# Kernel optimization log

Hardware: AMD Instinct MI355X
Metric: run time of the kernel (lower is better)

## Reference

```python
import jax, jax.numpy as jnp
import numpy as np

N_NODES = 100000
N_EDGES = 1600000
F_IN = 128
HID = 128
N_GRAPHS = 2048


def setup_inputs() -> dict:
    key = jax.random.key(0)
    ks = jax.random.split(key, 12)
    x = jax.random.normal(ks[0], (N_NODES, F_IN), dtype=jnp.float32)
    edge_index = jax.random.randint(ks[1], (2, N_EDGES), 0, N_NODES, dtype=jnp.int64)
    batch = jnp.sort(jax.random.randint(ks[2], (N_NODES,), 0, N_GRAPHS, dtype=jnp.int64))
    def glorot(k, fan_in, fan_out):
        s = jnp.sqrt(6.0 / (fan_in + fan_out)).astype(jnp.float32)
        return jax.random.uniform(k, (fan_in, fan_out), jnp.float32, -s, s)
    W1 = glorot(ks[3], F_IN, HID); b1 = jnp.zeros((HID,), jnp.float32)
    W2 = glorot(ks[4], HID, HID);  b2 = jnp.zeros((HID,), jnp.float32)
    W3 = glorot(ks[5], HID, HID);  b3 = jnp.zeros((HID,), jnp.float32)
    W4 = glorot(ks[6], HID, HID);  b4 = jnp.zeros((HID,), jnp.float32)
    return {"x": x, "W1": W1, "b1": b1, "W2": W2, "b2": b2,
            "W3": W3, "b3": b3, "W4": W4, "b4": b4,
            "edge_index": edge_index, "batch": batch}


def _gcn_norm(edge_index, n_nodes):
    # add self-loops, symmetric normalization: norm_e = d^{-1/2}[row] * d^{-1/2}[col]
    loop = jnp.arange(n_nodes, dtype=edge_index.dtype)
    row = jnp.concatenate([edge_index[0], loop])  # source
    col = jnp.concatenate([edge_index[1], loop])  # target
    deg = jax.ops.segment_sum(jnp.ones_like(col, dtype=jnp.float32), col,
                              num_segments=n_nodes)
    dis = jnp.where(deg > 0, jax.lax.rsqrt(jnp.maximum(deg, 1.0)), 0.0)
    norm = dis[row] * dis[col]
    return row, col, norm


def _gcn_conv(x, W, b, row, col, norm, n_nodes):
    h = x @ W                                   # [N, d_out]
    msg = norm[:, None] * h[row]                # gather + scale, [E+N, d_out]
    out = jax.ops.segment_sum(msg, col, num_segments=n_nodes)
    return out + b


def reference(x, W1, b1, W2, b2, W3, b3, W4, b4, edge_index, batch):
    n = x.shape[0]
    row, col, norm = _gcn_norm(edge_index, n)
    h = jax.nn.relu(_gcn_conv(x, W1, b1, row, col, norm, n))
    h = jax.nn.relu(_gcn_conv(h, W2, b2, row, col, norm, n))
    h = jax.nn.relu(_gcn_conv(h, W3, b3, row, col, norm, n))
    h = jax.nn.relu(_gcn_conv(h, W4, b4, row, col, norm, n))
    # global mean pool over graphs in the batch
    sums = jax.ops.segment_sum(h, batch, num_segments=N_GRAPHS)
    cnts = jax.ops.segment_sum(jnp.ones((n,), jnp.float32), batch,
                               num_segments=N_GRAPHS)
    return sums / jnp.maximum(cnts, 1.0)[:, None]
```

## Files before the change

kernel.cpp:

```cpp
#include <hip/hip_runtime.h>
#include <hip/hip_bf16.h>
#include <hip/hip_fp16.h>

typedef _Float16 half8 __attribute__((ext_vector_type(8)));
typedef _Float16 h2    __attribute__((ext_vector_type(2)));
typedef float    f32x4 __attribute__((ext_vector_type(4)));


__global__ void count_deg_k(const int* __restrict__ col,
                            unsigned int* __restrict__ deg, int E) {
    int e = blockIdx.x * blockDim.x + threadIdx.x;
    if (e < E) atomicAdd(&deg[col[e]], 1u);
}

__global__ void dis_k(const unsigned int* __restrict__ deg,
                      float* __restrict__ dis, int N) {
    int i = blockIdx.x * blockDim.x + threadIdx.x;
    if (i < N) dis[i] = rsqrtf((float)(deg[i] + 1u));
}

__global__ void scan1_k(const unsigned int* __restrict__ deg,
                        int* __restrict__ out, int* __restrict__ bsum, int N) {
    __shared__ int lds[256];
    int t = threadIdx.x;
    int base = blockIdx.x * 1024 + t * 4;
    int v0 = (base + 0 < N) ? (int)deg[base + 0] : 0;
    int v1 = (base + 1 < N) ? (int)deg[base + 1] : 0;
    int v2 = (base + 2 < N) ? (int)deg[base + 2] : 0;
    int v3 = (base + 3 < N) ? (int)deg[base + 3] : 0;
    lds[t] = v0 + v1 + v2 + v3;
    __syncthreads();
    for (int off = 1; off < 256; off <<= 1) {
        int x = lds[t];
        int y = (t >= off) ? lds[t - off] : 0;
        __syncthreads();
        lds[t] = x + y;
        __syncthreads();
    }
    int excl = (t == 0) ? 0 : lds[t - 1];
    if (base + 0 < N) out[base + 0] = excl;
    excl += v0;
    if (base + 1 < N) out[base + 1] = excl;
    excl += v1;
    if (base + 2 < N) out[base + 2] = excl;
    excl += v2;
    if (base + 3 < N) out[base + 3] = excl;
    if (t == 255) bsum[blockIdx.x] = lds[255];
}

__global__ void scan2_k(const int* __restrict__ bsum, int* __restrict__ boff, int nb) {
    __shared__ int lds[256];
    int t = threadIdx.x;
    lds[t] = (t < nb) ? bsum[t] : 0;
    __syncthreads();
    for (int off = 1; off < 256; off <<= 1) {
        int x = lds[t];
        int y = (t >= off) ? lds[t - off] : 0;
        __syncthreads();
        lds[t] = x + y;
        __syncthreads();
    }
    boff[t] = (t == 0) ? 0 : lds[t - 1];
}

__global__ void scan3_k(int* __restrict__ row_ptr, int* __restrict__ cursor,
                        const int* __restrict__ boff, int N, int E) {
    int i = blockIdx.x * blockDim.x + threadIdx.x;
    if (i < N) {
        int v = row_ptr[i] + boff[i >> 10];
        row_ptr[i] = v;
        cursor[i]  = v;
    }
    if (i == N) row_ptr[N] = E;
}

__global__ void fill_k(const int* __restrict__ row,
                       const int* __restrict__ col,
                       int* __restrict__ cursor, int* __restrict__ csr_row, int E) {
    int e = blockIdx.x * blockDim.x + threadIdx.x;
    if (e < E) {
        int c = col[e];
        int p = atomicAdd(&cursor[c], 1);
        csr_row[p] = row[e];
    }
}

__global__ void cnt_k(const int* __restrict__ batch,
                      unsigned int* __restrict__ cnt, int N) {
    int i = blockIdx.x * blockDim.x + threadIdx.x;
    if (i < N) atomicAdd(&cnt[batch[i]], 1u);
}

__global__ void wtcast_k(const float* __restrict__ W, _Float16* __restrict__ Wt) {
    int t = blockIdx.x * 256 + threadIdx.x;
    int k = t >> 7, n = t & 127;
    Wt[n * 128 + k] = (_Float16)W[t];
}

template<bool F32IN>
__global__ __launch_bounds__(256) void gemm_mfma_k(const void* __restrict__ Ain,
                                                   const _Float16* __restrict__ Wt,
                                                   const float* __restrict__ dis,
                                                   _Float16* __restrict__ H, int N) {
    int wave = threadIdx.x >> 6, l = threadIdx.x & 63;
    int lr = l & 15, lk = l >> 4;
    int row0 = blockIdx.x * 128 + wave * 32;

    half8 a[2][4];
#pragma unroll
    for (int m = 0; m < 2; ++m) {
#pragma unroll
        for (int s = 0; s < 4; ++s) {
            int r = row0 + m * 16 + lr;
            int k0 = s * 32 + lk * 8;
            half8 t;
            if (r < N) {
                if constexpr (F32IN) {
                    const float* ap = (const float*)Ain + (size_t)r * 128 + k0;
                    float4 u0 = *(const float4*)ap;
                    float4 u1 = *(const float4*)(ap + 4);
                    t[0] = (_Float16)u0.x; t[1] = (_Float16)u0.y;
                    t[2] = (_Float16)u0.z; t[3] = (_Float16)u0.w;
                    t[4] = (_Float16)u1.x; t[5] = (_Float16)u1.y;
                    t[6] = (_Float16)u1.z; t[7] = (_Float16)u1.w;
                } else {
                    t = *(const half8*)((const _Float16*)Ain + (size_t)r * 128 + k0);
                }
            } else {
#pragma unroll
                for (int i = 0; i < 8; ++i) t[i] = (_Float16)0.0f;
            }
            a[m][s] = t;
        }
    }

    f32x4 acc[2][8];
#pragma unroll
    for (int m = 0; m < 2; ++m)
#pragma unroll
        for (int nt = 0; nt < 8; ++nt)
#pragma unroll
            for (int r = 0; r < 4; ++r) acc[m][nt][r] = 0.0f;

#pragma unroll
    for (int nt = 0; nt < 8; ++nt) {
        half8 b[4];
#pragma unroll
        for (int s = 0; s < 4; ++s)
            b[s] = *(const half8*)(Wt + (size_t)(nt * 16 + lr) * 128 + s * 32 + lk * 8);
#pragma unroll
        for (int m = 0; m < 2; ++m)
#pragma unroll
            for (int s = 0; s < 4; ++s)
                acc[m][nt] = __builtin_amdgcn_mfma_f32_16x16x32_f16(a[m][s], b[s],
                                                                    acc[m][nt], 0, 0, 0);
    }

#pragma unroll
    for (int m = 0; m < 2; ++m) {
        int   orow[4];
        float dv[4];
#pragma unroll
        for (int r = 0; r < 4; ++r) {
            orow[r] = row0 + m * 16 + lk * 4 + r;
            dv[r]   = (orow[r] < N) ? dis[orow[r]] : 0.0f;
        }
#pragma unroll
        for (int nt = 0; nt < 8; ++nt)
#pragma unroll
            for (int r = 0; r < 4; ++r)
                if (orow[r] < N)
                    H[(size_t)orow[r] * 128 + nt * 16 + lr] =
                        (_Float16)(acc[m][nt][r] * dv[r]);
    }
}

template<bool POOL>
__global__ __launch_bounds__(256) void agg_h_k(const _Float16* __restrict__ Hd,
                                               const int* __restrict__ row_ptr,
                                               const int* __restrict__ csr_row,
                                               const float* __restrict__ dis,
                                               const float* __restrict__ bias,
                                               _Float16* __restrict__ Hout,
                                               const int* __restrict__ batch,
                                               float* __restrict__ pout, int N) {
    int wid  = (int)((blockIdx.x * (size_t)blockDim.x + threadIdx.x) >> 6);
    int lane = threadIdx.x & 63;
    if (wid >= N) return;
    int beg = row_ptr[wid], end = row_ptr[wid + 1];
    float di = dis[wid];
    const _Float16* hp = Hd + lane * 2;

    h2 self = *(const h2*)(hp + (size_t)wid * 128);
    float ax = (float)self[0], ay = (float)self[1];

    int j = beg;
    for (; j + 4 <= end; j += 4) {
        int s0 = csr_row[j], s1 = csr_row[j + 1], s2 = csr_row[j + 2], s3 = csr_row[j + 3];
        h2 v0 = *(const h2*)(hp + (size_t)s0 * 128);
        h2 v1 = *(const h2*)(hp + (size_t)s1 * 128);
        h2 v2 = *(const h2*)(hp + (size_t)s2 * 128);
        h2 v3 = *(const h2*)(hp + (size_t)s3 * 128);
        ax += (float)v0[0] + (float)v1[0] + (float)v2[0] + (float)v3[0];
        ay += (float)v0[1] + (float)v1[1] + (float)v2[1] + (float)v3[1];
    }
    for (; j < end; ++j) {
        int s = csr_row[j];
        h2 v = *(const h2*)(hp + (size_t)s * 128);
        ax += (float)v[0];
        ay += (float)v[1];
    }

    float bx = bias[lane * 2], by = bias[lane * 2 + 1];
    float ox = fmaxf(fmaf(di, ax, bx), 0.0f);
    float oy = fmaxf(fmaf(di, ay, by), 0.0f);

    if constexpr (POOL) {
        int g = batch[wid];
        atomicAdd(&pout[(size_t)g * 128 + lane * 2 + 0], ox);
        atomicAdd(&pout[(size_t)g * 128 + lane * 2 + 1], oy);
    } else {
        h2 o;
        o[0] = (_Float16)ox;
        o[1] = (_Float16)oy;
        *(h2*)(Hout + (size_t)wid * 128 + lane * 2) = o;
    }
}

__global__ void fin_k(float* __restrict__ out, const unsigned int* __restrict__ cnt,
                      int total) {
    int i = blockIdx.x * blockDim.x + threadIdx.x;
    if (i < total) out[i] = out[i] / fmaxf((float)cnt[i >> 7], 1.0f);
}

extern "C" void kernel_launch(void* const* d_in, const int* in_sizes, int n_in,
                              void* d_out, int out_size, void* d_ws, size_t ws_size,
                              hipStream_t stream) {
    const float* x  = (const float*)d_in[0];
    const float* W1 = (const float*)d_in[1]; const float* b1 = (const float*)d_in[2];
    const float* W2 = (const float*)d_in[3]; const float* b2 = (const float*)d_in[4];
    const float* W3 = (const float*)d_in[5]; const float* b3 = (const float*)d_in[6];
    const float* W4 = (const float*)d_in[7]; const float* b4 = (const float*)d_in[8];
    const int* eidx  = (const int*)d_in[9];
    const int* batch = (const int*)d_in[10];

    int N = in_sizes[0] / 128;
    int E = in_sizes[9] / 2;
    const int* erow = eidx;
    const int* ecol = eidx + E;

    char* ws = (char*)d_ws;
    size_t off = 0;
    auto alloc = [&](size_t bytes) -> void* {
        void* p = ws + off;
        off = (off + bytes + 255) & ~(size_t)255;
        return p;
    };
    unsigned int* deg    = (unsigned int*)alloc((size_t)N * 4);
    float*        dis    = (float*)alloc((size_t)N * 4);
    int*          rowp   = (int*)alloc((size_t)(N + 1) * 4);
    int*          cursor = (int*)alloc((size_t)N * 4);
    int*          bsum   = (int*)alloc(1024);
    int*          boff   = (int*)alloc(1024);
    unsigned int* cnt    = (unsigned int*)alloc(2048 * 4);
    int*          csr    = (int*)alloc((size_t)E * 4);
    _Float16*     Wt1    = (_Float16*)alloc(128 * 128 * 2);
    _Float16*     Wt2    = (_Float16*)alloc(128 * 128 * 2);
    _Float16*     Wt3    = (_Float16*)alloc(128 * 128 * 2);
    _Float16*     Wt4    = (_Float16*)alloc(128 * 128 * 2);
    _Float16*     hA     = (_Float16*)alloc((size_t)N * 128 * 2);
    _Float16*     hB     = (_Float16*)alloc((size_t)N * 128 * 2);
    (void)ws_size;

    hipMemsetAsync(deg, 0, (size_t)N * 4, stream);
    hipMemsetAsync(cnt, 0, 2048 * 4, stream);
    hipMemsetAsync(d_out, 0, (size_t)out_size * 4, stream);

    const int B = 256;
    count_deg_k<<<(E + B - 1) / B, B, 0, stream>>>(ecol, deg, E);
    dis_k<<<(N + B - 1) / B, B, 0, stream>>>(deg, dis, N);
    int nb = (N + 1023) / 1024;
    scan1_k<<<nb, 256, 0, stream>>>(deg, rowp, bsum, N);
    scan2_k<<<1, 256, 0, stream>>>(bsum, boff, nb);
    scan3_k<<<(N + 1 + B - 1) / B, B, 0, stream>>>(rowp, cursor, boff, N, E);
    fill_k<<<(E + B - 1) / B, B, 0, stream>>>(erow, ecol, cursor, csr, E);
    cnt_k<<<(N + B - 1) / B, B, 0, stream>>>(batch, cnt, N);
    wtcast_k<<<64, 256, 0, stream>>>(W1, Wt1);
    wtcast_k<<<64, 256, 0, stream>>>(W2, Wt2);
    wtcast_k<<<64, 256, 0, stream>>>(W3, Wt3);
    wtcast_k<<<64, 256, 0, stream>>>(W4, Wt4);

    int gb = (N + 127) / 128;
    int ab = (N + 3) / 4;

    gemm_mfma_k<true ><<<gb, 256, 0, stream>>>(x,  Wt1, dis, hA, N);
    agg_h_k<false><<<ab, 256, 0, stream>>>(hA, rowp, csr, dis, b1, hB, batch, nullptr, N);
    gemm_mfma_k<false><<<gb, 256, 0, stream>>>(hB, Wt2, dis, hA, N);
    agg_h_k<false><<<ab, 256, 0, stream>>>(hA, rowp, csr, dis, b2, hB, batch, nullptr, N);
    gemm_mfma_k<false><<<gb, 256, 0, stream>>>(hB, Wt3, dis, hA, N);
    agg_h_k<false><<<ab, 256, 0, stream>>>(hA, rowp, csr, dis, b3, hB, batch, nullptr, N);
    gemm_mfma_k<false><<<gb, 256, 0, stream>>>(hB, Wt4, dis, hA, N);
    agg_h_k<true ><<<ab, 256, 0, stream>>>(hA, rowp, csr, dis, b4, nullptr, batch,
                                           (float*)d_out, N);

    fin_k<<<(out_size + B - 1) / B, B, 0, stream>>>((float*)d_out, cnt, out_size);
}
```

Before: 774.6 us.

## Fuse aggregation with next layer GEMM and merge setup kernels

Each layer's neighbour aggregation is now fused with the following layer's MFMA GEMM: a block aggregates 64 nodes into shared memory, then multiplies by the next weight matrix and writes the scaled result. This removes the intermediate activation write and re-read and the separate GEMM launches. Setup kernels are also merged: degree and batch counting share one kernel, dis is computed inside the scan, and the four weight casts become one launch. The fused kernel processes 16 nodes serially per wave with fewer blocks, which may reduce latency hiding in the gather phase.

```diff
diff --git a/kernel.cpp b/kernel.cpp
--- a/kernel.cpp
+++ b/kernel.cpp
@@ -7,20 +7,17 @@
 typedef float    f32x4 __attribute__((ext_vector_type(4)));
 
 
-__global__ void count_deg_k(const int* __restrict__ col,
-                            unsigned int* __restrict__ deg, int E) {
+__global__ void count2_k(const int* __restrict__ col, unsigned int* __restrict__ deg,
+                         const int* __restrict__ batch, unsigned int* __restrict__ cnt,
+                         int E, int N) {
     int e = blockIdx.x * blockDim.x + threadIdx.x;
     if (e < E) atomicAdd(&deg[col[e]], 1u);
-}
-
-__global__ void dis_k(const unsigned int* __restrict__ deg,
-                      float* __restrict__ dis, int N) {
-    int i = blockIdx.x * blockDim.x + threadIdx.x;
-    if (i < N) dis[i] = rsqrtf((float)(deg[i] + 1u));
+    if (e < N) atomicAdd(&cnt[batch[e]], 1u);
 }
 
 __global__ void scan1_k(const unsigned int* __restrict__ deg,
-                        int* __restrict__ out, int* __restrict__ bsum, int N) {
+                        int* __restrict__ out, int* __restrict__ bsum,
+                        float* __restrict__ dis, int N) {
     __shared__ int lds[256];
     int t = threadIdx.x;
     int base = blockIdx.x * 1024 + t * 4;
@@ -28,6 +25,10 @@
     int v1 = (base + 1 < N) ? (int)deg[base + 1] : 0;
     int v2 = (base + 2 < N) ? (int)deg[base + 2] : 0;
     int v3 = (base + 3 < N) ? (int)deg[base + 3] : 0;
+    if (base + 0 < N) dis[base + 0] = rsqrtf((float)(v0 + 1));
+    if (base + 1 < N) dis[base + 1] = rsqrtf((float)(v1 + 1));
+    if (base + 2 < N) dis[base + 2] = rsqrtf((float)(v2 + 1));
+    if (base + 3 < N) dis[base + 3] = rsqrtf((float)(v3 + 1));
     lds[t] = v0 + v1 + v2 + v3;
     __syncthreads();
     for (int off = 1; off < 256; off <<= 1) {
@@ -81,27 +82,24 @@
     if (e < E) {
         int c = col[e];
         int p = atomicAdd(&cursor[c], 1);
-        csr_row[p] = row[e];
-    }
-}
-
-__global__ void cnt_k(const int* __restrict__ batch,
-                      unsigned int* __restrict__ cnt, int N) {
-    int i = blockIdx.x * blockDim.x + threadIdx.x;
-    if (i < N) atomicAdd(&cnt[batch[i]], 1u);
-}
-
-__global__ void wtcast_k(const float* __restrict__ W, _Float16* __restrict__ Wt) {
+        __builtin_nontemporal_store(row[e], &csr_row[p]);
+    }
+}
+
+__global__ void wtcast4_k(const float* __restrict__ W1, const float* __restrict__ W2,
+                          const float* __restrict__ W3, const float* __restrict__ W4,
+                          _Float16* __restrict__ Wt) {
     int t = blockIdx.x * 256 + threadIdx.x;
-    int k = t >> 7, n = t & 127;
-    Wt[n * 128 + k] = (_Float16)W[t];
-}
-
-template<bool F32IN>
-__global__ __launch_bounds__(256) void gemm_mfma_k(const void* __restrict__ Ain,
-                                                   const _Float16* __restrict__ Wt,
-                                                   const float* __restrict__ dis,
-                                                   _Float16* __restrict__ H, int N) {
+    int w = t >> 14, idx = t & 16383;
+    int k = idx >> 7, n = idx & 127;
+    const float* W = (w == 0) ? W1 : (w == 1) ? W2 : (w == 2) ? W3 : W4;
+    Wt[(size_t)w * 16384 + n * 128 + k] = (_Float16)W[idx];
+}
+
+__global__ __launch_bounds__(256) void gemm1_k(const float* __restrict__ X,
+                                               const _Float16* __restrict__ Wt,
+                                               const float* __restrict__ dis,
+                                               _Float16* __restrict__ H, int N) {
     int wave = threadIdx.x >> 6, l = threadIdx.x & 63;
     int lr = l & 15, lk = l >> 4;
     int row0 = blockIdx.x * 128 + wave * 32;
@@ -115,17 +113,13 @@
             int k0 = s * 32 + lk * 8;
             half8 t;
             if (r < N) {
-                if constexpr (F32IN) {
-                    const float* ap = (const float*)Ain + (size_t)r * 128 + k0;
-                    float4 u0 = *(const float4*)ap;
-                    float4 u1 = *(const float4*)(ap + 4);
-                    t[0] = (_Float16)u0.x; t[1] = (_Float16)u0.y;
-                    t[2] = (_Float16)u0.z; t[3] = (_Float16)u0.w;
-                    t[4] = (_Float16)u1.x; t[5] = (_Float16)u1.y;
-                    t[6] = (_Float16)u1.z; t[7] = (_Float16)u1.w;
-                } else {
-                    t = *(const half8*)((const _Float16*)Ain + (size_t)r * 128 + k0);
-                }
+                const float* ap = X + (size_t)r * 128 + k0;
+                float4 u0 = *(const float4*)ap;
+                float4 u1 = *(const float4*)(ap + 4);
+                t[0] = (_Float16)u0.x; t[1] = (_Float16)u0.y;
+                t[2] = (_Float16)u0.z; t[3] = (_Float16)u0.w;
+                t[4] = (_Float16)u1.x; t[5] = (_Float16)u1.y;
+                t[6] = (_Float16)u1.z; t[7] = (_Float16)u1.w;
             } else {
 #pragma unroll
                 for (int i = 0; i < 8; ++i) t[i] = (_Float16)0.0f;
@@ -175,15 +169,101 @@
     }
 }
 
-template<bool POOL>
-__global__ __launch_bounds__(256) void agg_h_k(const _Float16* __restrict__ Hd,
+__global__ __launch_bounds__(256) void fused_k(const _Float16* __restrict__ Tin,
                                                const int* __restrict__ row_ptr,
                                                const int* __restrict__ csr_row,
                                                const float* __restrict__ dis,
                                                const float* __restrict__ bias,
-                                               _Float16* __restrict__ Hout,
-                                               const int* __restrict__ batch,
-                                               float* __restrict__ pout, int N) {
+                                               const _Float16* __restrict__ Wt,
+                                               _Float16* __restrict__ Tout, int N) {
+    __shared__ _Float16 S[64][136];
+    int wave = threadIdx.x >> 6, l = threadIdx.x & 63;
+    int node0 = blockIdx.x * 64;
+    float bx = bias[l * 2], by = bias[l * 2 + 1];
+    const _Float16* hp = Tin + l * 2;
+
+#pragma unroll 1
+    for (int i = 0; i < 16; ++i) {
+        int nl = wave * 16 + i;
+        int nd = node0 + nl;
+        float ox = 0.0f, oy = 0.0f;
+        if (nd < N) {
+            int beg = row_ptr[nd], end = row_ptr[nd + 1];
+            float di = dis[nd];
+            h2 self = *(const h2*)(hp + (size_t)nd * 128);
+            float ax = (float)self[0], ay = (float)self[1];
+            int j = beg;
+            for (; j + 4 <= end; j += 4) {
+                int s0 = csr_row[j],     s1 = csr_row[j + 1];
+                int s2 = csr_row[j + 2], s3 = csr_row[j + 3];
+                h2 v0 = *(const h2*)(hp + (size_t)s0 * 128);
+                h2 v1 = *(const h2*)(hp + (size_t)s1 * 128);
+                h2 v2 = *(const h2*)(hp + (size_t)s2 * 128);
+                h2 v3 = *(const h2*)(hp + (size_t)s3 * 128);
+                ax += (float)v0[0] + (float)v1[0] + (float)v2[0] + (float)v3[0];
+                ay += (float)v0[1] + (float)v1[1] + (float)v2[1] + (float)v3[1];
+            }
+            for (; j < end; ++j) {
+                int s = csr_row[j];
+                h2 v = *(const h2*)(hp + (size_t)s * 128);
+                ax += (float)v[0];
+                ay += (float)v[1];
+            }
+            ox = fmaxf(fmaf(di, ax, bx), 0.0f);
+            oy = fmaxf(fmaf(di, ay, by), 0.0f);
+        }
+        h2 o;
+        o[0] = (_Float16)ox;
+        o[1] = (_Float16)oy;
+        *(h2*)&S[nl][l * 2] = o;
+    }
+
+    int lr = l & 15, lk = l >> 4;
+    half8 a[4];
+#pragma unroll
+    for (int s = 0; s < 4; ++s)
+        a[s] = *(const half8*)&S[wave * 16 + lr][s * 32 + lk * 8];
+
+    f32x4 acc[8];
+#pragma unroll
+    for (int nt = 0; nt < 8; ++nt)
+#pragma unroll
+        for (int r = 0; r < 4; ++r) acc[nt][r] = 0.0f;
+
+#pragma unroll
+    for (int nt = 0; nt < 8; ++nt) {
+        half8 b[4];
+#pragma unroll
+        for (int s = 0; s < 4; ++s)
+            b[s] = *(const half8*)(Wt + (size_t)(nt * 16 + lr) * 128 + s * 32 + lk * 8);
+#pragma unroll
+        for (int s = 0; s < 4; ++s)
+            acc[nt] = __builtin_amdgcn_mfma_f32_16x16x32_f16(a[s], b[s], acc[nt], 0, 0, 0);
+    }
+
+    int   orow[4];
+    float dv[4];
+#pragma unroll
+    for (int r = 0; r < 4; ++r) {
+        orow[r] = node0 + wave * 16 + lk * 4 + r;
+        dv[r]   = (orow[r] < N) ? dis[orow[r]] : 0.0f;
+    }
+#pragma unroll
+    for (int nt = 0; nt < 8; ++nt)
+#pragma unroll
+        for (int r = 0; r < 4; ++r)
+            if (orow[r] < N)
+                Tout[(size_t)orow[r] * 128 + nt * 16 + lr] =
+                    (_Float16)(acc[nt][r] * dv[r]);
+}
+
+__global__ __launch_bounds__(256) void agg_pool_k(const _Float16* __restrict__ Hd,
+                                                  const int* __restrict__ row_ptr,
+                                                  const int* __restrict__ csr_row,
+                                                  const float* __restrict__ dis,
+                                                  const float* __restrict__ bias,
+                                                  const int* __restrict__ batch,
+                                                  float* __restrict__ pout, int N) {
     int wid  = (int)((blockIdx.x * (size_t)blockDim.x + threadIdx.x) >> 6);
     int lane = threadIdx.x & 63;
     if (wid >= N) return;
@@ -211,20 +291,11 @@
         ay += (float)v[1];
     }
 
-    float bx = bias[lane * 2], by = bias[lane * 2 + 1];
-    float ox = fmaxf(fmaf(di, ax, bx), 0.0f);
-    float oy = fmaxf(fmaf(di, ay, by), 0.0f);
-
-    if constexpr (POOL) {
-        int g = batch[wid];
-        atomicAdd(&pout[(size_t)g * 128 + lane * 2 + 0], ox);
-        atomicAdd(&pout[(size_t)g * 128 + lane * 2 + 1], oy);
-    } else {
-        h2 o;
-        o[0] = (_Float16)ox;
-        o[1] = (_Float16)oy;
-        *(h2*)(Hout + (size_t)wid * 128 + lane * 2) = o;
-    }
+    float ox = fmaxf(fmaf(di, ax, bias[lane * 2]),     0.0f);
+    float oy = fmaxf(fmaf(di, ay, bias[lane * 2 + 1]), 0.0f);
+    int g = batch[wid];
+    atomicAdd(&pout[(size_t)g * 128 + lane * 2 + 0], ox);
+    atomicAdd(&pout[(size_t)g * 128 + lane * 2 + 1], oy);
 }
 
 __global__ void fin_k(float* __restrict__ out, const unsigned int* __restrict__ cnt,
@@ -264,10 +335,7 @@
     int*          boff   = (int*)alloc(1024);
     unsigned int* cnt    = (unsigned int*)alloc(2048 * 4);
     int*          csr    = (int*)alloc((size_t)E * 4);
-    _Float16*     Wt1    = (_Float16*)alloc(128 * 128 * 2);
-    _Float16*     Wt2    = (_Float16*)alloc(128 * 128 * 2);
-    _Float16*     Wt3    = (_Float16*)alloc(128 * 128 * 2);
-    _Float16*     Wt4    = (_Float16*)alloc(128 * 128 * 2);
+    _Float16*     Wt     = (_Float16*)alloc(4 * 128 * 128 * 2);
     _Float16*     hA     = (_Float16*)alloc((size_t)N * 128 * 2);
     _Float16*     hB     = (_Float16*)alloc((size_t)N * 128 * 2);
     (void)ws_size;
@@ -277,31 +345,23 @@
     hipMemsetAsync(d_out, 0, (size_t)out_size * 4, stream);
 
     const int B = 256;
-    count_deg_k<<<(E + B - 1) / B, B, 0, stream>>>(ecol, deg, E);
-    dis_k<<<(N + B - 1) / B, B, 0, stream>>>(deg, dis, N);
+    count2_k<<<(E + B - 1) / B, B, 0, stream>>>(ecol, deg, batch, cnt, E, N);
     int nb = (N + 1023) / 1024;
-    scan1_k<<<nb, 256, 0, stream>>>(deg, rowp, bsum, N);
+    scan1_k<<<nb, 256, 0, stream>>>(deg, rowp, bsum, dis, N);
     scan2_k<<<1, 256, 0, stream>>>(bsum, boff, nb);
     scan3_k<<<(N + 1 + B - 1) / B, B, 0, stream>>>(rowp, cursor, boff, N, E);
     fill_k<<<(E + B - 1) / B, B, 0, stream>>>(erow, ecol, cursor, csr, E);
-    cnt_k<<<(N + B - 1) / B, B, 0, stream>>>(batch, cnt, N);
-    wtcast_k<<<64, 256, 0, stream>>>(W1, Wt1);
-    wtcast_k<<<64, 256, 0, stream>>>(W2, Wt2);
-    wtcast_k<<<64, 256, 0, stream>>>(W3, Wt3);
-    wtcast_k<<<64, 256, 0, stream>>>(W4, Wt4);
+    wtcast4_k<<<256, 256, 0, stream>>>(W1, W2, W3, W4, Wt);
 
     int gb = (N + 127) / 128;
+    int fb = (N + 63) / 64;
     int ab = (N + 3) / 4;
 
-    gemm_mfma_k<true ><<<gb, 256, 0, stream>>>(x,  Wt1, dis, hA, N);
-    agg_h_k<false><<<ab, 256, 0, stream>>>(hA, rowp, csr, dis, b1, hB, batch, nullptr, N);
-    gemm_mfma_k<false><<<gb, 256, 0, stream>>>(hB, Wt2, dis, hA, N);
-    agg_h_k<false><<<ab, 256, 0, stream>>>(hA, rowp, csr, dis, b2, hB, batch, nullptr, N);
-    gemm_mfma_k<false><<<gb, 256, 0, stream>>>(hB, Wt3, dis, hA, N);
-    agg_h_k<false><<<ab, 256, 0, stream>>>(hA, rowp, csr, dis, b3, hB, batch, nullptr, N);
-    gemm_mfma_k<false><<<gb, 256, 0, stream>>>(hB, Wt4, dis, hA, N);
-    agg_h_k<true ><<<ab, 256, 0, stream>>>(hA, rowp, csr, dis, b4, nullptr, batch,
-                                           (float*)d_out, N);
-
+    gemm1_k<<<gb, 256, 0, stream>>>(x, Wt, dis, hA, N);
+    fused_k<<<fb, 256, 0, stream>>>(hA, rowp, csr, dis, b1, Wt + 16384, hB, N);
+    fused_k<<<fb, 256, 0, stream>>>(hB, rowp, csr, dis, b2, Wt + 32768, hA, N);
+    fused_k<<<fb, 256, 0, stream>>>(hA, rowp, csr, dis, b3, Wt + 49152, hB, N);
+    agg_pool_k<<<ab, 256, 0, stream>>>(hB, rowp, csr, dis, b4, batch,
+                                       (float*)d_out, N);
     fin_k<<<(out_size + B - 1) / B, B, 0, stream>>>((float*)d_out, cnt, out_size);
 }
```

Measured after the change: 920.7 us. +18.9%, slower.

## Split wave into four edge groups with 16-byte gathers; merge small setup kernels

Applied to the files above, without the earlier changes.

The aggregation kernel now splits each wave into four 16-lane groups. Each group gathers a full 256-byte neighbor row with 16-byte loads and handles a different edge, and the partial sums are reduced with cross-lane shuffles. Previously all 64 lanes did 4-byte loads on the same edge. Several setup kernels are also merged: degree and batch counting share one kernel, the dis computation moves into the scan, and the four weight casts run as one launch. The CSR fill now uses nontemporal stores. This is meant to cut gather instruction count, raise memory-level parallelism and remove launch overhead, at the cost of a shuffle reduction and idle lanes for low-degree tails.

```diff
diff --git a/kernel.cpp b/kernel.cpp
--- a/kernel.cpp
+++ b/kernel.cpp
@@ -7,20 +7,17 @@
 typedef float    f32x4 __attribute__((ext_vector_type(4)));
 
 
-__global__ void count_deg_k(const int* __restrict__ col,
-                            unsigned int* __restrict__ deg, int E) {
+__global__ void count2_k(const int* __restrict__ col, unsigned int* __restrict__ deg,
+                         const int* __restrict__ batch, unsigned int* __restrict__ cnt,
+                         int E, int N) {
     int e = blockIdx.x * blockDim.x + threadIdx.x;
     if (e < E) atomicAdd(&deg[col[e]], 1u);
-}
-
-__global__ void dis_k(const unsigned int* __restrict__ deg,
-                      float* __restrict__ dis, int N) {
-    int i = blockIdx.x * blockDim.x + threadIdx.x;
-    if (i < N) dis[i] = rsqrtf((float)(deg[i] + 1u));
+    if (e < N) atomicAdd(&cnt[batch[e]], 1u);
 }
 
 __global__ void scan1_k(const unsigned int* __restrict__ deg,
-                        int* __restrict__ out, int* __restrict__ bsum, int N) {
+                        int* __restrict__ out, int* __restrict__ bsum,
+                        float* __restrict__ dis, int N) {
     __shared__ int lds[256];
     int t = threadIdx.x;
     int base = blockIdx.x * 1024 + t * 4;
@@ -28,6 +25,10 @@
     int v1 = (base + 1 < N) ? (int)deg[base + 1] : 0;
     int v2 = (base + 2 < N) ? (int)deg[base + 2] : 0;
     int v3 = (base + 3 < N) ? (int)deg[base + 3] : 0;
+    if (base + 0 < N) dis[base + 0] = rsqrtf((float)(v0 + 1));
+    if (base + 1 < N) dis[base + 1] = rsqrtf((float)(v1 + 1));
+    if (base + 2 < N) dis[base + 2] = rsqrtf((float)(v2 + 1));
+    if (base + 3 < N) dis[base + 3] = rsqrtf((float)(v3 + 1));
     lds[t] = v0 + v1 + v2 + v3;
     __syncthreads();
     for (int off = 1; off < 256; off <<= 1) {
@@ -81,20 +82,18 @@
     if (e < E) {
         int c = col[e];
         int p = atomicAdd(&cursor[c], 1);
-        csr_row[p] = row[e];
-    }
-}
-
-__global__ void cnt_k(const int* __restrict__ batch,
-                      unsigned int* __restrict__ cnt, int N) {
-    int i = blockIdx.x * blockDim.x + threadIdx.x;
-    if (i < N) atomicAdd(&cnt[batch[i]], 1u);
-}
-
-__global__ void wtcast_k(const float* __restrict__ W, _Float16* __restrict__ Wt) {
+        __builtin_nontemporal_store(row[e], &csr_row[p]);
+    }
+}
+
+__global__ void wtcast4_k(const float* __restrict__ W1, const float* __restrict__ W2,
+                          const float* __restrict__ W3, const float* __restrict__ W4,
+                          _Float16* __restrict__ Wt) {
     int t = blockIdx.x * 256 + threadIdx.x;
-    int k = t >> 7, n = t & 127;
-    Wt[n * 128 + k] = (_Float16)W[t];
+    int w = t >> 14, idx = t & 16383;
+    int k = idx >> 7, n = idx & 127;
+    const float* W = (w == 0) ? W1 : (w == 1) ? W2 : (w == 2) ? W3 : W4;
+    Wt[(size_t)w * 16384 + n * 128 + k] = (_Float16)W[idx];
 }
 
 template<bool F32IN>
@@ -176,54 +175,73 @@
 }
 
 template<bool POOL>
-__global__ __launch_bounds__(256) void agg_h_k(const _Float16* __restrict__ Hd,
-                                               const int* __restrict__ row_ptr,
-                                               const int* __restrict__ csr_row,
-                                               const float* __restrict__ dis,
-                                               const float* __restrict__ bias,
-                                               _Float16* __restrict__ Hout,
-                                               const int* __restrict__ batch,
-                                               float* __restrict__ pout, int N) {
+__global__ __launch_bounds__(256) void agg4_k(const _Float16* __restrict__ Hd,
+                                              const int* __restrict__ row_ptr,
+                                              const int* __restrict__ csr_row,
+                                              const float* __restrict__ dis,
+                                              const float* __restrict__ bias,
+                                              _Float16* __restrict__ Hout,
+                                              const int* __restrict__ batch,
+                                              float* __restrict__ pout, int N) {
     int wid  = (int)((blockIdx.x * (size_t)blockDim.x + threadIdx.x) >> 6);
     int lane = threadIdx.x & 63;
     if (wid >= N) return;
+    int a = lane >> 4, b = lane & 15;
+    const _Float16* hp = Hd + b * 8;
+
+    float acc[8];
+    if (a == 0) {
+        half8 s = *(const half8*)(hp + (size_t)wid * 128);
+#pragma unroll
+        for (int f = 0; f < 8; ++f) acc[f] = (float)s[f];
+    } else {
+#pragma unroll
+        for (int f = 0; f < 8; ++f) acc[f] = 0.0f;
+    }
+
     int beg = row_ptr[wid], end = row_ptr[wid + 1];
-    float di = dis[wid];
-    const _Float16* hp = Hd + lane * 2;
-
-    h2 self = *(const h2*)(hp + (size_t)wid * 128);
-    float ax = (float)self[0], ay = (float)self[1];
-
     int j = beg;
-    for (; j + 4 <= end; j += 4) {
-        int s0 = csr_row[j], s1 = csr_row[j + 1], s2 = csr_row[j + 2], s3 = csr_row[j + 3];
-        h2 v0 = *(const h2*)(hp + (size_t)s0 * 128);
-        h2 v1 = *(const h2*)(hp + (size_t)s1 * 128);
-        h2 v2 = *(const h2*)(hp + (size_t)s2 * 128);
-        h2 v3 = *(const h2*)(hp + (size_t)s3 * 128);
-        ax += (float)v0[0] + (float)v1[0] + (float)v2[0] + (float)v3[0];
-        ay += (float)v0[1] + (float)v1[1] + (float)v2[1] + (float)v3[1];
-    }
-    for (; j < end; ++j) {
-        int s = csr_row[j];
-        h2 v = *(const h2*)(hp + (size_t)s * 128);
-        ax += (float)v[0];
-        ay += (float)v[1];
-    }
-
-    float bx = bias[lane * 2], by = bias[lane * 2 + 1];
-    float ox = fmaxf(fmaf(di, ax, bx), 0.0f);
-    float oy = fmaxf(fmaf(di, ay, by), 0.0f);
-
-    if constexpr (POOL) {
-        int g = batch[wid];
-        atomicAdd(&pout[(size_t)g * 128 + lane * 2 + 0], ox);
-        atomicAdd(&pout[(size_t)g * 128 + lane * 2 + 1], oy);
-    } else {
-        h2 o;
-        o[0] = (_Float16)ox;
-        o[1] = (_Float16)oy;
-        *(h2*)(Hout + (size_t)wid * 128 + lane * 2) = o;
+    for (; j + 8 <= end; j += 8) {
+        int s0 = csr_row[j + a];
+        int s1 = csr_row[j + 4 + a];
+        half8 v0 = *(const half8*)(hp + (size_t)s0 * 128);
+        half8 v1 = *(const half8*)(hp + (size_t)s1 * 128);
+#pragma unroll
+        for (int f = 0; f < 8; ++f) acc[f] += (float)v0[f] + (float)v1[f];
+    }
+    for (; j < end; j += 4) {
+        int idx = j + a;
+        if (idx < end) {
+            int s = csr_row[idx];
+            half8 v = *(const half8*)(hp + (size_t)s * 128);
+#pragma unroll
+            for (int f = 0; f < 8; ++f) acc[f] += (float)v[f];
+        }
+    }
+
+#pragma unroll
+    for (int f = 0; f < 8; ++f) {
+        acc[f] += __shfl_xor(acc[f], 16, 64);
+        acc[f] += __shfl_xor(acc[f], 32, 64);
+    }
+
+    if (a == 0) {
+        float di = dis[wid];
+        float o[8];
+#pragma unroll
+        for (int f = 0; f < 8; ++f)
+            o[f] = fmaxf(fmaf(di, acc[f], bias[b * 8 + f]), 0.0f);
+        if constexpr (POOL) {
+            int g = batch[wid];
+#pragma unroll
+            for (int f = 0; f < 8; ++f)
+                atomicAdd(&pout[(size_t)g * 128 + b * 8 + f], o[f]);
+        } else {
+            half8 ov;
+#pragma unroll
+            for (int f = 0; f < 8; ++f) ov[f] = (_Float16)o[f];
+            *(half8*)(Hout + (size_t)wid * 128 + b * 8) = ov;
+        }
     }
 }
 
@@ -264,10 +282,7 @@
     int*          boff   = (int*)alloc(1024);
     unsigned int* cnt    = (unsigned int*)alloc(2048 * 4);
     int*          csr    = (int*)alloc((size_t)E * 4);
-    _Float16*     Wt1    = (_Float16*)alloc(128 * 128 * 2);
-    _Float16*     Wt2    = (_Float16*)alloc(128 * 128 * 2);
-    _Float16*     Wt3    = (_Float16*)alloc(128 * 128 * 2);
-    _Float16*     Wt4    = (_Float16*)alloc(128 * 128 * 2);
+    _Float16*     Wt     = (_Float16*)alloc(4 * 128 * 128 * 2);
     _Float16*     hA     = (_Float16*)alloc((size_t)N * 128 * 2);
     _Float16*     hB     = (_Float16*)alloc((size_t)N * 128 * 2);
     (void)ws_size;
@@ -277,31 +292,26 @@
     hipMemsetAsync(d_out, 0, (size_t)out_size * 4, stream);
 
     const int B = 256;
-    count_deg_k<<<(E + B - 1) / B, B, 0, stream>>>(ecol, deg, E);
-    dis_k<<<(N + B - 1) / B, B, 0, stream>>>(deg, dis, N);
+    count2_k<<<(E + B - 1) / B, B, 0, stream>>>(ecol, deg, batch, cnt, E, N);
     int nb = (N + 1023) / 1024;
-    scan1_k<<<nb, 256, 0, stream>>>(deg, rowp, bsum, N);
+    scan1_k<<<nb, 256, 0, stream>>>(deg, rowp, bsum, dis, N);
     scan2_k<<<1, 256, 0, stream>>>(bsum, boff, nb);
     scan3_k<<<(N + 1 + B - 1) / B, B, 0, stream>>>(rowp, cursor, boff, N, E);
     fill_k<<<(E + B - 1) / B, B, 0, stream>>>(erow, ecol, cursor, csr, E);
-    cnt_k<<<(N + B - 1) / B, B, 0, stream>>>(batch, cnt, N);
-    wtcast_k<<<64, 256, 0, stream>>>(W1, Wt1);
-    wtcast_k<<<64, 256, 0, stream>>>(W2, Wt2);
-    wtcast_k<<<64, 256, 0, stream>>>(W3, Wt3);
-    wtcast_k<<<64, 256, 0, stream>>>(W4, Wt4);
+    wtcast4_k<<<256, 256, 0, stream>>>(W1, W2, W3, W4, Wt);
 
     int gb = (N + 127) / 128;
     int ab = (N + 3) / 4;
 
-    gemm_mfma_k<true ><<<gb, 256, 0, stream>>>(x,  Wt1, dis, hA, N);
-    agg_h_k<false><<<ab, 256, 0, stream>>>(hA, rowp, csr, dis, b1, hB, batch, nullptr, N);
-    gemm_mfma_k<false><<<gb, 256, 0, stream>>>(hB, Wt2, dis, hA, N);
-    agg_h_k<false><<<ab, 256, 0, stream>>>(hA, rowp, csr, dis, b2, hB, batch, nullptr, N);
-    gemm_mfma_k<false><<<gb, 256, 0, stream>>>(hB, Wt3, dis, hA, N);
-    agg_h_k<false><<<ab, 256, 0, stream>>>(hA, rowp, csr, dis, b3, hB, batch, nullptr, N);
-    gemm_mfma_k<false><<<gb, 256, 0, stream>>>(hB, Wt4, dis, hA, N);
-    agg_h_k<true ><<<ab, 256, 0, stream>>>(hA, rowp, csr, dis, b4, nullptr, batch,
-                                           (float*)d_out, N);
+    gemm_mfma_k<true ><<<gb, 256, 0, stream>>>(x, Wt, dis, hA, N);
+    agg4_k<false><<<ab, 256, 0, stream>>>(hA, rowp, csr, dis, b1, hB, batch, nullptr, N);
+    gemm_mfma_k<false><<<gb, 256, 0, stream>>>(hB, Wt + 16384, dis, hA, N);
+    agg4_k<false><<<ab, 256, 0, stream>>>(hA, rowp, csr, dis, b2, hB, batch, nullptr, N);
+    gemm_mfma_k<false><<<gb, 256, 0, stream>>>(hB, Wt + 32768, dis, hA, N);
+    agg4_k<false><<<ab, 256, 0, stream>>>(hA, rowp, csr, dis, b3, hB, batch, nullptr, N);
+    gemm_mfma_k<false><<<gb, 256, 0, stream>>>(hB, Wt + 49152, dis, hA, N);
+    agg4_k<true ><<<ab, 256, 0, stream>>>(hA, rowp, csr, dis, b4, nullptr, batch,
+                                          (float*)d_out, N);
 
     fin_k<<<(out_size + B - 1) / B, B, 0, stream>>>((float*)d_out, cnt, out_size);
 }
```

New measurement: 1.031 ms. 33.1% more time.
